# Performance work log

Measured on AMD Instinct MI355X. Metric: run time of the kernel, lower is better.

The kernel has to match this reference:

```python
import jax, jax.numpy as jnp
import numpy as np

B, D_IN, HID, DEPTH = 16384, 128, 16, 8
N_INNER = 2 ** DEPTH - 1   # 255
N_LEAF = 2 ** DEPTH        # 256


def setup_inputs() -> dict:
    key = jax.random.key(0)
    ks = jax.random.split(key, 4)
    x = jax.random.normal(ks[0], (B, D_IN), jnp.float32)
    # Batched per-inner-node tiny MLP parameters (PyTorch stores one Sequential per node;
    # we stack them along a leading node axis so the math is identical but vectorized).
    W1 = jax.random.normal(ks[1], (N_INNER, D_IN, HID), jnp.float32) / np.sqrt(D_IN).astype(np.float32)
    b1 = jnp.zeros((N_INNER, HID), jnp.float32)
    W2 = jax.random.normal(ks[2], (N_INNER, HID), jnp.float32) / np.sqrt(HID).astype(np.float32)
    b2 = jnp.zeros((N_INNER,), jnp.float32)
    leaf = jax.random.normal(ks[3], (N_LEAF, 1), jnp.float32) * 0.1
    return {"x": x, "W1": W1, "b1": b1, "W2": W2, "b2": b2, "leaf": leaf}


def reference(x, W1, b1, W2, b2, leaf):
    b = x.shape[0]
    depth = int(np.log2(leaf.shape[0]))
    # All inner-node gates in one batched GEMM: p[b, n] = sigmoid(W2_n . relu(W1_n^T x_b + b1_n) + b2_n)
    h1 = jax.nn.relu(jnp.einsum('bi,nih->bnh', x, W1) + b1[None])  # [B, N_inner, hid]
    p = jax.nn.sigmoid(jnp.einsum('bnh,nh->bn', h1, W2) + b2[None])  # [B, N_inner]

    # Level-by-level probability propagation (heap-ordered nodes):
    # children of node j are 2j+1 (left, mass*(1-p)) and 2j+2 (right, mass*p).
    r = jnp.ones((b, 1), x.dtype)
    levels = []
    for l in range(depth):
        levels.append(r)
        pl = p[:, 2 ** l - 1: 2 ** (l + 1) - 1]  # probs of nodes at level l, [B, 2^l]
        # interleave (left, right) so child ordering matches heap indexing
        r = jnp.stack([r * (1.0 - pl), r * pl], axis=-1).reshape(b, 2 ** (l + 1))
    node_reach = jnp.concatenate(levels, axis=1)  # [B, N_inner]
    path_probs = r                                 # [B, N_leaf]

    h = (path_probs @ leaf)[:, 0]                  # [B]
    return (h, path_probs, p, node_reach)
```

## Files before the change

kernel.cpp:

```cpp
#include <hip/hip_runtime.h>

#define BATCH 16384
#define DIN   128
#define HIDN  16
#define NNODE 255
#define NLEAF 256

typedef _Float16 half8 __attribute__((ext_vector_type(8)));
typedef float   float4v __attribute__((ext_vector_type(4)));

__global__ __launch_bounds__(256) void k_pack(const float* __restrict__ x, const float* __restrict__ w1,
                                              half8* __restrict__ xp, half8* __restrict__ w1p) {
    __shared__ float w[DIN * 17];
    int t = threadIdx.x;
    if (blockIdx.x < 1024) {
        int gid  = blockIdx.x * 256 + t;
        int lane = gid & 63;
        int kc   = (gid >> 6) & 3;
        int bt   = gid >> 8;
        const float4* src = (const float4*)(x + (size_t)(bt * 16 + (lane & 15)) * DIN + kc * 32 + ((lane >> 4) * 8));
        float4 v0 = src[0], v1 = src[1];
        half8 v;
        v[0] = (_Float16)v0.x; v[1] = (_Float16)v0.y; v[2] = (_Float16)v0.z; v[3] = (_Float16)v0.w;
        v[4] = (_Float16)v1.x; v[5] = (_Float16)v1.y; v[6] = (_Float16)v1.z; v[7] = (_Float16)v1.w;
        xp[gid] = v;
    } else {
        int n = blockIdx.x - 1024;
        const float4* src = (const float4*)(w1 + (size_t)n * (DIN * HIDN)) + t * 2;
        float4 a0 = src[0], a1 = src[1];
        int base = t * 8;
#pragma unroll
        for (int e = 0; e < 4; ++e) {
            int idx0 = base + e, idx1 = base + 4 + e;
            w[(idx0 >> 4) * 17 + (idx0 & 15)] = (&a0.x)[e];
            w[(idx1 >> 4) * 17 + (idx1 & 15)] = (&a1.x)[e];
        }
        __syncthreads();
        int L  = t & 63;
        int kc = t >> 6;
        int m  = L & 15;
        int k0 = kc * 32 + (L >> 4) * 8;
        half8 v;
#pragma unroll
        for (int j = 0; j < 8; ++j) v[j] = (_Float16)w[(k0 + j) * 17 + m];
        w1p[(size_t)n * 256 + t] = v;
    }
}

__global__ __launch_bounds__(768, 3) void k_fused(const half8* __restrict__ xp, const half8* __restrict__ w1p,
                                                  const float* __restrict__ b1, const float* __restrict__ w2,
                                                  const float* __restrict__ b2, const float* __restrict__ leaf,
                                                  float* __restrict__ h_out, float* __restrict__ pp_out,
                                                  float* __restrict__ p_out, float* __restrict__ nr_out) {
    __shared__ float sp[64][260];
    int wv   = threadIdx.x >> 6;
    int lane = threadIdx.x & 63;
    int q    = lane >> 4;
    int bt0  = blockIdx.x * 4;

    half8 bq[4][4];
#pragma unroll
    for (int t = 0; t < 4; ++t)
#pragma unroll
        for (int kc = 0; kc < 4; ++kc)
            bq[t][kc] = xp[(size_t)((bt0 + t) * 4 + kc) * 64 + lane];
    asm volatile("" ::: "memory");

    half8  aA[4], aB[4];
    float4 b1A, b1B, w2A, w2B;
    float  b2A, b2B;

    int nA = wv;
#pragma unroll
    for (int kc = 0; kc < 4; ++kc) aA[kc] = w1p[(size_t)(nA * 4 + kc) * 64 + lane];
    b1A = ((const float4*)(b1 + nA * HIDN))[q];
    w2A = ((const float4*)(w2 + nA * HIDN))[q];
    b2A = b2[nA];
    {
        int nB = nA + 12;
#pragma unroll
        for (int kc = 0; kc < 4; ++kc) aB[kc] = w1p[(size_t)(nB * 4 + kc) * 64 + lane];
        b1B = ((const float4*)(b1 + nB * HIDN))[q];
        w2B = ((const float4*)(w2 + nB * HIDN))[q];
        b2B = b2[nB];
    }

#define MLP_BODY(AS, B1S, W2S, B2S, NODE, PREN)                                            \
    do {                                                                                   \
        float4v acc0 = {B1S.x, B1S.y, B1S.z, B1S.w};                                       \
        float4v acc1 = acc0, acc2 = acc0, acc3 = acc0;                                     \
        _Pragma("unroll") for (int kc = 0; kc < 4; ++kc) {                                 \
            acc0 = __builtin_amdgcn_mfma_f32_16x16x32_f16(AS[kc], bq[0][kc], acc0, 0, 0, 0);\
            acc1 = __builtin_amdgcn_mfma_f32_16x16x32_f16(AS[kc], bq[1][kc], acc1, 0, 0, 0);\
            acc2 = __builtin_amdgcn_mfma_f32_16x16x32_f16(AS[kc], bq[2][kc], acc2, 0, 0, 0);\
            acc3 = __builtin_amdgcn_mfma_f32_16x16x32_f16(AS[kc], bq[3][kc], acc3, 0, 0, 0);\
        }                                                                                  \
        float s0 = fmaf(fmaxf(acc0[0], 0.f), W2S.x, fmaf(fmaxf(acc0[1], 0.f), W2S.y,       \
                   fmaf(fmaxf(acc0[2], 0.f), W2S.z, fmaxf(acc0[3], 0.f) * W2S.w)));        \
        float s1 = fmaf(fmaxf(acc1[0], 0.f), W2S.x, fmaf(fmaxf(acc1[1], 0.f), W2S.y,       \
                   fmaf(fmaxf(acc1[2], 0.f), W2S.z, fmaxf(acc1[3], 0.f) * W2S.w)));        \
        float s2 = fmaf(fmaxf(acc2[0], 0.f), W2S.x, fmaf(fmaxf(acc2[1], 0.f), W2S.y,       \
                   fmaf(fmaxf(acc2[2], 0.f), W2S.z, fmaxf(acc2[3], 0.f) * W2S.w)));        \
        float s3 = fmaf(fmaxf(acc3[0], 0.f), W2S.x, fmaf(fmaxf(acc3[1], 0.f), W2S.y,       \
                   fmaf(fmaxf(acc3[2], 0.f), W2S.z, fmaxf(acc3[3], 0.f) * W2S.w)));        \
        float b2c = B2S;                                                                   \
        _Pragma("unroll") for (int kc = 0; kc < 4; ++kc)                                   \
            AS[kc] = w1p[(size_t)((PREN) * 4 + kc) * 64 + lane];                           \
        B1S = ((const float4*)(b1 + (PREN) * HIDN))[q];                                    \
        W2S = ((const float4*)(w2 + (PREN) * HIDN))[q];                                    \
        B2S = b2[PREN];                                                                    \
        int q1 = q & 1, q2 = q & 2;                                                        \
        float a01 = q1 ? s1 : s0, c01 = q1 ? s0 : s1;                                      \
        a01 += __shfl_xor(c01, 16, 64);                                                    \
        float a23 = q1 ? s3 : s2, c23 = q1 ? s2 : s3;                                      \
        a23 += __shfl_xor(c23, 16, 64);                                                    \
        float e = q2 ? a23 : a01, f = q2 ? a01 : a23;                                      \
        e += __shfl_xor(f, 32, 64);                                                        \
        float lg = e + b2c;                                                                \
        sp[lane][NODE] =                                                                   \
            __builtin_amdgcn_rcpf(1.f + __builtin_amdgcn_exp2f(-1.44269504088896f * lg));  \
    } while (0)

    for (int ii = 0; ii < 11; ++ii) {
        int pA = nA + 24; pA = pA > 254 ? 254 : pA;
        MLP_BODY(aA, b1A, w2A, b2A, nA, pA);
        int nB = nA + 12; nB = nB > 254 ? 254 : nB;
        int pB = nA + 36; pB = pB > 254 ? 254 : pB;
        MLP_BODY(aB, b1B, w2B, b2B, nB, pB);
        nA += 24;
    }
#undef MLP_BODY
    __syncthreads();

    const float4 lf = *(const float4*)(leaf + 4 * lane);
    for (int r = wv; r < 64; r += 12) {
        int b = blockIdx.x * 64 + r;
        const float* P = &sp[r][0];
        float* nr = nr_out + (size_t)b * NNODE;

#pragma unroll
        for (int c = 0; c < 4; ++c) {
            int idx = c * 64 + lane;
            if (idx < NNODE)
                p_out[(size_t)b * NNODE + idx] = P[idx];
        }

        float pref = 1.f;
#pragma unroll
        for (int l = 0; l < 6; ++l) {
            if ((lane & ((1 << (6 - l)) - 1)) == 0)
                nr[(1 << l) - 1 + (lane >> (6 - l))] = pref;
            float pv  = P[(1 << l) - 1 + (lane >> (6 - l))];
            int  bit  = (lane >> (5 - l)) & 1;
            pref *= bit ? pv : (1.f - pv);
        }
        nr[63 + lane] = pref;
        float p6 = P[63 + lane];
        float pl = pref * (1.f - p6);
        float pr = pref * p6;
        nr[127 + 2 * lane] = pl;
        nr[128 + 2 * lane] = pr;
        float p7a = P[127 + 2 * lane];
        float p7b = P[128 + 2 * lane];
        float4v pp;
        pp[0] = pl * (1.f - p7a);
        pp[1] = pl * p7a;
        pp[2] = pr * (1.f - p7b);
        pp[3] = pr * p7b;
        *(float4v*)(pp_out + (size_t)b * NLEAF + 4 * lane) = pp;
        float hs = pp[0] * lf.x + pp[1] * lf.y + pp[2] * lf.z + pp[3] * lf.w;
#pragma unroll
        for (int off = 1; off < 64; off <<= 1) hs += __shfl_xor(hs, off, 64);
        if (lane == 0) h_out[b] = hs;
    }
}

extern "C" void kernel_launch(void* const* d_in, const int* in_sizes, int n_in,
                              void* d_out, int out_size, void* d_ws, size_t ws_size,
                              hipStream_t stream) {
    const float* x    = (const float*)d_in[0];
    const float* W1   = (const float*)d_in[1];
    const float* b1   = (const float*)d_in[2];
    const float* W2   = (const float*)d_in[3];
    const float* b2   = (const float*)d_in[4];
    const float* leaf = (const float*)d_in[5];

    float* out    = (float*)d_out;
    float* h_out  = out;
    float* pp_out = out + BATCH;
    float* p_out  = pp_out + (size_t)BATCH * NLEAF;
    float* nr_out = p_out + (size_t)BATCH * NNODE;

    half8* xp  = (half8*)d_ws;
    half8* w1p = xp + (size_t)1024 * 4 * 64;

    hipLaunchKernelGGL(k_pack,  dim3(1024 + NNODE), dim3(256), 0, stream, x, W1, xp, w1p);
    hipLaunchKernelGGL(k_fused, dim3(256),          dim3(768), 0, stream,
                       xp, w1p, b1, W2, b2, leaf, h_out, pp_out, p_out, nr_out);
}
```

Before: 106.6 us.

## Split fused kernel into MLP and tree-propagation kernels via node-major workspace

The fused kernel is split in two. The MLP kernel now writes gate probabilities to a node-major global workspace instead of shared memory. A new tree kernel with many small blocks (16 rows each) transposes these through LDS and writes p, node_reach, path_probs and h. The aim is to spread the output-heavy tree phase over many more blocks than the original 256, and to free the MLP kernel from the large LDS buffer. In exchange it adds an extra launch and a full round trip of the probability matrix through global memory.

```diff
diff --git a/kernel.cpp b/kernel.cpp
--- a/kernel.cpp
+++ b/kernel.cpp
@@ -5,6 +5,7 @@
 #define HIDN  16
 #define NNODE 255
 #define NLEAF 256
+#define TR    16
 
 typedef _Float16 half8 __attribute__((ext_vector_type(8)));
 typedef float   float4v __attribute__((ext_vector_type(4)));
@@ -47,16 +48,14 @@
     }
 }
 
-__global__ __launch_bounds__(768, 3) void k_fused(const half8* __restrict__ xp, const half8* __restrict__ w1p,
-                                                  const float* __restrict__ b1, const float* __restrict__ w2,
-                                                  const float* __restrict__ b2, const float* __restrict__ leaf,
-                                                  float* __restrict__ h_out, float* __restrict__ pp_out,
-                                                  float* __restrict__ p_out, float* __restrict__ nr_out) {
-    __shared__ float sp[64][260];
-    int wv   = threadIdx.x >> 6;
-    int lane = threadIdx.x & 63;
-    int q    = lane >> 4;
-    int bt0  = blockIdx.x * 4;
+__global__ __launch_bounds__(768, 3) void k_mlp(const half8* __restrict__ xp, const half8* __restrict__ w1p,
+                                                const float* __restrict__ b1, const float* __restrict__ w2,
+                                                const float* __restrict__ b2, float* __restrict__ p_ws) {
+    int wv    = threadIdx.x >> 6;
+    int lane  = threadIdx.x & 63;
+    int q     = lane >> 4;
+    int bt0   = blockIdx.x * 4;
+    int bbase = blockIdx.x * 64 + lane;
 
     half8 bq[4][4];
 #pragma unroll
@@ -117,7 +116,7 @@
         float e = q2 ? a23 : a01, f = q2 ? a01 : a23;                                      \
         e += __shfl_xor(f, 32, 64);                                                        \
         float lg = e + b2c;                                                                \
-        sp[lane][NODE] =                                                                   \
+        p_ws[(size_t)(NODE) * BATCH + bbase] =                                             \
             __builtin_amdgcn_rcpf(1.f + __builtin_amdgcn_exp2f(-1.44269504088896f * lg));  \
     } while (0)
 
@@ -130,26 +129,43 @@
         nA += 24;
     }
 #undef MLP_BODY
+}
+
+__global__ __launch_bounds__(256) void k_tree(const float* __restrict__ p_ws, const float* __restrict__ leaf,
+                                              float* __restrict__ h_out, float* __restrict__ pp_out,
+                                              float* __restrict__ p_out, float* __restrict__ nr_out) {
+    __shared__ float sp[TR][NNODE + 2];
+    int wv   = threadIdx.x >> 6;
+    int lane = threadIdx.x & 63;
+    int b0   = blockIdx.x * TR;
+    int t    = threadIdx.x;
+
+#pragma unroll
+    for (int i = 0; i < 4; ++i) {
+        int idx = i * 256 + t;
+        if (idx < NNODE * 4) {
+            int n = idx >> 2, b4 = (idx & 3) * 4;
+            const float4 v = *(const float4*)(p_ws + (size_t)n * BATCH + b0 + b4);
+            sp[b4 + 0][n] = v.x; sp[b4 + 1][n] = v.y; sp[b4 + 2][n] = v.z; sp[b4 + 3][n] = v.w;
+        }
+    }
     __syncthreads();
 
+    for (int r = 0; r < TR; ++r)
+        if (t < NNODE)
+            p_out[(size_t)(b0 + r) * NNODE + t] = sp[r][t];
+
     const float4 lf = *(const float4*)(leaf + 4 * lane);
-    for (int r = wv; r < 64; r += 12) {
-        int b = blockIdx.x * 64 + r;
-        const float* P = &sp[r][0];
+    for (int rr = 0; rr < 4; ++rr) {
+        int i = wv * 4 + rr;
+        int b = b0 + i;
+        const float* P = &sp[i][0];
         float* nr = nr_out + (size_t)b * NNODE;
 
-#pragma unroll
-        for (int c = 0; c < 4; ++c) {
-            int idx = c * 64 + lane;
-            if (idx < NNODE)
-                p_out[(size_t)b * NNODE + idx] = P[idx];
-        }
-
         float pref = 1.f;
 #pragma unroll
         for (int l = 0; l < 6; ++l) {
-            if ((lane & ((1 << (6 - l)) - 1)) == 0)
-                nr[(1 << l) - 1 + (lane >> (6 - l))] = pref;
+            if ((lane & ((1 << (6 - l)) - 1)) == 0) nr[(1 << l) - 1 + (lane >> (6 - l))] = pref;
             float pv  = P[(1 << l) - 1 + (lane >> (6 - l))];
             int  bit  = (lane >> (5 - l)) & 1;
             pref *= bit ? pv : (1.f - pv);
@@ -191,10 +207,12 @@
     float* p_out  = pp_out + (size_t)BATCH * NLEAF;
     float* nr_out = p_out + (size_t)BATCH * NNODE;
 
-    half8* xp  = (half8*)d_ws;
-    half8* w1p = xp + (size_t)1024 * 4 * 64;
-
-    hipLaunchKernelGGL(k_pack,  dim3(1024 + NNODE), dim3(256), 0, stream, x, W1, xp, w1p);
-    hipLaunchKernelGGL(k_fused, dim3(256),          dim3(768), 0, stream,
-                       xp, w1p, b1, W2, b2, leaf, h_out, pp_out, p_out, nr_out);
-}
+    half8* xp   = (half8*)d_ws;
+    half8* w1p  = xp + (size_t)1024 * 4 * 64;
+    float* p_ws = (float*)(w1p + (size_t)NNODE * 256);
+
+    hipLaunchKernelGGL(k_pack, dim3(1024 + NNODE), dim3(256), 0, stream, x, W1, xp, w1p);
+    hipLaunchKernelGGL(k_mlp,  dim3(256),          dim3(768), 0, stream, xp, w1p, b1, W2, b2, p_ws);
+    hipLaunchKernelGGL(k_tree, dim3(BATCH / TR),   dim3(256), 0, stream,
+                       p_ws, leaf, h_out, pp_out, p_out, nr_out);
+}
```

After: 119.8 us. 12.4% more time.
